# Kernel optimization log

Hardware: AMD Instinct MI355X
Metric: run time of the kernel (lower is better)

The kernel has to match this reference:

```python
import jax, jax.numpy as jnp
import numpy as np


def setup_inputs() -> dict:
    key = jax.random.key(0)
    k1, k2, k3, k4 = jax.random.split(key, 4)
    b, n1, n2, h = 8, 2048, 2048, 1024
    scale = 1.0 / np.sqrt(h)
    return {
        "S1": jax.random.normal(k1, (b, n1, h), dtype=jnp.float32),
        "S2": jax.random.normal(k2, (b, n2, h), dtype=jnp.float32),
        "W1": jax.random.normal(k3, (h, h), dtype=jnp.float32) * scale,
        "W2": jax.random.normal(k4, (h, h), dtype=jnp.float32) * scale,
    }


def reference(S1, S2, W1, W2):
    # nn.Linear(h, h, bias=False): y = x @ W.T
    S2_h = jnp.einsum('bnh,kh->bnk', S2, W1)            # (b, N2, h)
    scores1 = jnp.einsum('bmh,bnh->bmn', S1, S2_h)      # (b, N1, N2)
    attn1 = jax.nn.softmax(scores1, axis=-1)
    S1_out = jnp.einsum('bmn,bnh->bmh', attn1, S2)      # (b, N1, h)

    S1_h = jnp.einsum('bmh,kh->bmk', S1, W2)            # (b, N1, h)
    scores2 = jnp.einsum('bnh,bmh->bnm', S2, S1_h)      # (b, N2, N1)
    attn2 = jax.nn.softmax(scores2, axis=-1)
    S2_out = jnp.einsum('bnm,bmh->bnh', attn2, S1)      # (b, N2, h)
    return (S1_out, S2_out)
```

## Files before the change

### kernel.cpp

```cpp
#include <hip/hip_runtime.h>

typedef _Float16 f16;
typedef _Float16 f16x4 __attribute__((ext_vector_type(4)));
typedef _Float16 f16x8 __attribute__((ext_vector_type(8)));
typedef float    f32x4 __attribute__((ext_vector_type(4)));

#define MFMA(a,b,c) __builtin_amdgcn_mfma_f32_16x16x32_f16(a,b,c,0,0,0)
#define SBAR() __builtin_amdgcn_sched_barrier(0)
#define BARRIER() do { SBAR(); __builtin_amdgcn_s_barrier(); SBAR(); } while (0)
#define VMCNT(n) do { SBAR(); asm volatile("s_waitcnt vmcnt(" #n ")" ::: "memory"); SBAR(); } while (0)

__device__ __forceinline__ void gload_lds16(const f16* g, f16* l) {
  __builtin_amdgcn_global_load_lds(
      (const __attribute__((address_space(1))) unsigned int*)g,
      (__attribute__((address_space(3))) unsigned int*)l, 16, 0, 0);
}

__global__ __launch_bounds__(256)
void tof16_kernel(const float* __restrict__ x, f16* __restrict__ y, int n4) {
  int i = blockIdx.x * 256 + threadIdx.x;
  if (i >= n4) return;
  f32x4 v = ((const f32x4*)x)[i];
  f16x4 h;
#pragma unroll
  for (int j = 0; j < 4; j++) h[j] = (f16)v[j];
  ((f16x4*)y)[i] = h;
}

__global__ __launch_bounds__(256)
void transpose_f16_kernel(const float* __restrict__ in, f16* __restrict__ out) {
  __shared__ f16 t[64][68];
  const int tid = threadIdx.x;
  const size_t z = blockIdx.z;
  const int n0 = blockIdx.x * 64, h0 = blockIdx.y * 64;
  const int rr = tid >> 4, cc = (tid & 15) * 4;
#pragma unroll
  for (int p = 0; p < 4; p++) {
    int n = rr + p * 16;
    f32x4 v = *(const f32x4*)(in + ((size_t)z * 2048 + n0 + n) * 1024 + h0 + cc);
    f16x4 h;
#pragma unroll
    for (int j = 0; j < 4; j++) h[j] = (f16)v[j];
    *(f16x4*)&t[n][cc] = h;
  }
  __syncthreads();
#pragma unroll
  for (int p = 0; p < 4; p++) {
    int h = rr + p * 16;
    f16x4 o;
#pragma unroll
    for (int j = 0; j < 4; j++) o[j] = t[cc + j][h];
    *(f16x4*)(out + ((size_t)z * 1024 + h0 + h) * 2048 + n0 + cc) = o;
  }
}

template <int OUTF32>
__global__ __launch_bounds__(512, 2)
void gemm256(const f16* __restrict__ Ag, size_t zA,
             const f16* __restrict__ Bg, size_t zB,
             void* __restrict__ Cg, size_t zC,
             int lda, int ldb, int ldc, int K, int gx) {
  __shared__ f16 sm[8][8192];
  const int tid = threadIdx.x;
  const size_t z = blockIdx.z;
  int bx = blockIdx.x;
  { int qq = gx >> 3; bx = (bx & 7) * qq + (bx >> 3); }
  const f16* A = Ag + z * zA + (size_t)bx * 256 * lda;
  const f16* B = Bg + z * zB + (size_t)blockIdx.y * 256 * ldb;

  const int lane = tid & 63, w = tid >> 6;
  const int wm = w >> 2, wn = w & 3;
  const int lr = lane & 15, kg = lane >> 4;
  const int sx = (kg ^ ((lr >> 1) & 3)) << 3;
  const int aoff = wm * 4096 + lr * 32 + sx;
  const int boff = wn * 2048 + lr * 32 + sx;
  const int colx = (((tid & 3) ^ ((tid >> 3) & 3)) << 3);
  const int srow = tid >> 2;
  const int wls = w * 512;

  f32x4 acc[8][4] = {};
  f16x8 af[8], bf0, bf1;

#define STAGE(cc, mat, kkv, ktc) do {                                          \
    const f16* gs = ((mat) ? B : A) + (size_t)srow * ((mat) ? ldb : lda) +     \
                    (ktc) + (kkv) * 32 + colx;                                 \
    f16* ls = &sm[(cc) * 4 + (mat) * 2 + (kkv)][wls];                          \
    gload_lds16(gs, ls);                                                       \
    gload_lds16(gs + (size_t)128 * ((mat) ? ldb : lda), ls + 4096);            \
  } while (0)

#define LOAD_A(cc, kkv) do { _Pragma("unroll")                                 \
    for (int fm = 0; fm < 8; fm++)                                             \
      af[fm] = *(const f16x8*)&sm[(cc) * 4 + (kkv)][aoff + fm * 512];          \
  } while (0)

#define LOAD_B(cc, kkv, nh) do {                                               \
    bf0 = *(const f16x8*)&sm[(cc) * 4 + 2 + (kkv)][boff + (nh) * 1024];        \
    bf1 = *(const f16x8*)&sm[(cc) * 4 + 2 + (kkv)][boff + (nh) * 1024 + 512];  \
  } while (0)

#define DOMFMA(nh) do {                                                        \
    __builtin_amdgcn_s_setprio(1);                                             \
    _Pragma("unroll")                                                          \
    for (int fm = 0; fm < 8; fm++) {                                           \
      acc[fm][(nh) * 2]     = MFMA(af[fm], bf0, acc[fm][(nh) * 2]);            \
      acc[fm][(nh) * 2 + 1] = MFMA(af[fm], bf1, acc[fm][(nh) * 2 + 1]);        \
    }                                                                          \
    __builtin_amdgcn_s_setprio(0);                                             \
    SBAR();                                                                    \
  } while (0)

  const int nt = K >> 6;
  STAGE(0, 0, 0, 0);
  STAGE(0, 1, 0, 0);
  STAGE(0, 0, 1, 0);
  STAGE(0, 1, 1, 0);

  for (int t = 0; t < nt - 1; ++t) {
    const int c = t & 1;
    const int kt1 = (t + 1) << 6;
    STAGE(c ^ 1, 0, 0, kt1);
    VMCNT(6);
    BARRIER();
    LOAD_A(c, 0); LOAD_B(c, 0, 0);
    DOMFMA(0);
    BARRIER();
    STAGE(c ^ 1, 1, 0, kt1);
    BARRIER();
    LOAD_B(c, 0, 1);
    DOMFMA(1);
    BARRIER();
    STAGE(c ^ 1, 0, 1, kt1);
    VMCNT(6);
    BARRIER();
    LOAD_A(c, 1); LOAD_B(c, 1, 0);
    DOMFMA(0);
    BARRIER();
    STAGE(c ^ 1, 1, 1, kt1);
    BARRIER();
    LOAD_B(c, 1, 1);
    DOMFMA(1);
    BARRIER();
  }
  {
    const int c = (nt - 1) & 1;
    VMCNT(4);
    BARRIER();
    LOAD_A(c, 0); LOAD_B(c, 0, 0);
    DOMFMA(0);
    BARRIER();
    LOAD_B(c, 0, 1);
    DOMFMA(1);
    VMCNT(0);
    BARRIER();
    LOAD_A(c, 1); LOAD_B(c, 1, 0);
    DOMFMA(0);
    BARRIER();
    LOAD_B(c, 1, 1);
    DOMFMA(1);
  }

#pragma unroll
  for (int fm = 0; fm < 8; fm++)
#pragma unroll
    for (int fn = 0; fn < 4; fn++)
#pragma unroll
      for (int q = 0; q < 4; q++) {
        size_t grow = (size_t)bx * 256 + wm * 128 + fm * 16 + kg * 4 + q;
        int gcol = blockIdx.y * 256 + wn * 64 + fn * 16 + lr;
        if (OUTF32)
          ((float*)Cg)[z * zC + grow * ldc + gcol] = acc[fm][fn][q];
        else
          ((f16*)Cg)[z * zC + grow * ldc + gcol] = (f16)acc[fm][fn][q];
      }
#undef STAGE
#undef LOAD_A
#undef LOAD_B
#undef DOMFMA
}

__global__ __launch_bounds__(256)
void softmax_rows(const float* __restrict__ SC, f16* __restrict__ Pb) {
  const float* r = SC + (size_t)blockIdx.x * 2048;
  f16* po = Pb + (size_t)blockIdx.x * 2048;
  const int tid = threadIdx.x;
  f32x4 a = *(const f32x4*)(r + tid * 8);
  f32x4 b = *(const f32x4*)(r + tid * 8 + 4);
  float x[8] = {a[0], a[1], a[2], a[3], b[0], b[1], b[2], b[3]};
#pragma unroll
  for (int i = 0; i < 8; i++) x[i] = fminf(fmaxf(x[i], -1e30f), 1e30f);
  float m = x[0];
#pragma unroll
  for (int i = 1; i < 8; i++) m = fmaxf(m, x[i]);
#pragma unroll
  for (int off = 32; off; off >>= 1) m = fmaxf(m, __shfl_xor(m, off));
  __shared__ float rmax[4], rsum[4];
  const int w = tid >> 6, lane = tid & 63;
  if (!lane) rmax[w] = m;
  __syncthreads();
  m = fmaxf(fmaxf(rmax[0], rmax[1]), fmaxf(rmax[2], rmax[3]));
  float e[8], s = 0.f;
#pragma unroll
  for (int i = 0; i < 8; i++) {
    e[i] = __expf(x[i] - m);
    s += e[i];
  }
#pragma unroll
  for (int off = 32; off; off >>= 1) s += __shfl_xor(s, off);
  if (!lane) rsum[w] = s;
  __syncthreads();
  s = rsum[0] + rsum[1] + rsum[2] + rsum[3];
  float inv = 1.0f / s;
  f16x8 p;
#pragma unroll
  for (int i = 0; i < 8; i++) p[i] = (f16)(e[i] * inv);
  *(f16x8*)(po + tid * 8) = p;
}

extern "C" void kernel_launch(void* const* d_in, const int* in_sizes, int n_in,
                              void* d_out, int out_size, void* d_ws, size_t ws_size,
                              hipStream_t stream) {
  const float* S1 = (const float*)d_in[0];
  const float* S2 = (const float*)d_in[1];
  const float* W1 = (const float*)d_in[2];
  const float* W2 = (const float*)d_in[3];
  float* out = (float*)d_out;
  const int B = 8, N = 2048, H = 1024;
  const size_t NH = (size_t)N * H;
  const size_t WN = (size_t)H * H;

  char* ws = (char*)d_ws;
  f16* W1h = (f16*)ws;
  f16* W2h = W1h + WN;
  size_t fixed = 2 * WN * sizeof(f16);
  size_t perb = 5 * NH * sizeof(f16) + (size_t)N * N * sizeof(float) +
                (size_t)N * N * sizeof(f16);

  int bc = 1;
  const int cands[4] = {8, 4, 2, 1};
  for (int ci = 0; ci < 4; ci++) {
    if (fixed + (size_t)cands[ci] * perb <= ws_size) { bc = cands[ci]; break; }
  }
  f16* Ah = (f16*)(ws + fixed);
  f16* Bh = Ah + (size_t)bc * NH;
  f16* At = Bh + (size_t)bc * NH;
  f16* Bt = At + (size_t)bc * NH;
  f16* Kh = Bt + (size_t)bc * NH;
  float* SC = (float*)(Kh + (size_t)bc * NH);
  f16* Pb = (f16*)(SC + (size_t)bc * N * N);

  {
    int n4 = (int)(WN / 4);
    tof16_kernel<<<dim3((n4 + 255) / 256), 256, 0, stream>>>(W1, W1h, n4);
    tof16_kernel<<<dim3((n4 + 255) / 256), 256, 0, stream>>>(W2, W2h, n4);
  }

  for (int c0 = 0; c0 < B; c0 += bc) {
    int n4 = (int)((size_t)bc * NH / 4);
    tof16_kernel<<<dim3((n4 + 255) / 256), 256, 0, stream>>>(S1 + (size_t)c0 * NH, Ah, n4);
    tof16_kernel<<<dim3((n4 + 255) / 256), 256, 0, stream>>>(S2 + (size_t)c0 * NH, Bh, n4);
    transpose_f16_kernel<<<dim3(N / 64, H / 64, bc), 256, 0, stream>>>(
        S1 + (size_t)c0 * NH, At);
    transpose_f16_kernel<<<dim3(N / 64, H / 64, bc), 256, 0, stream>>>(
        S2 + (size_t)c0 * NH, Bt);

    for (int path = 0; path < 2; path++) {
      const f16* Qh = path ? Bh : Ah;
      const f16* Xh = path ? Ah : Bh;
      const f16* Vt = path ? At : Bt;
      const f16* Wh = path ? W2h : W1h;
      float* Op = out + (size_t)path * B * NH + (size_t)c0 * NH;

      gemm256<0><<<dim3(bc * N / 256, H / 256, 1), 512, 0, stream>>>(
          Xh, 0, Wh, 0, Kh, 0, H, H, H, H, bc * N / 256);
      gemm256<1><<<dim3(N / 256, N / 256, bc), 512, 0, stream>>>(
          Qh, NH, Kh, NH, SC, (size_t)N * N, H, H, N, H, N / 256);
      softmax_rows<<<dim3(bc * N), 256, 0, stream>>>(SC, Pb);
      gemm256<1><<<dim3(N / 256, H / 256, bc), 512, 0, stream>>>(
          Pb, (size_t)N * N, Vt, NH, Op, NH, N, N, H, N, N / 256);
    }
  }
}
```

Before: 537.0 us.

## Reorder GEMM main loop to overlap LDS fragment loads with staging and fuse prep kernels

Restructures the gemm256 K-loop so LDS fragment reads are issued before the next global-to-LDS stage, with explicit lgkmcnt waits before the MFMA blocks and the vmcnt waits moved to the end of each half-iteration. The aim is to hide LDS read latency behind global load issue. Separately, the f16 conversion and transpose of S1/S2 are fused into one prep kernel that writes both row-major and transposed copies, which removes a full pass over the f32 inputs. The added barriers in the epilogue and the reordering risk extra synchronization stalls and correctness hazards around LDS buffer reuse.

```diff
diff --git a/kernel.cpp b/kernel.cpp
--- a/kernel.cpp
+++ b/kernel.cpp
@@ -9,6 +9,7 @@
 #define SBAR() __builtin_amdgcn_sched_barrier(0)
 #define BARRIER() do { SBAR(); __builtin_amdgcn_s_barrier(); SBAR(); } while (0)
 #define VMCNT(n) do { SBAR(); asm volatile("s_waitcnt vmcnt(" #n ")" ::: "memory"); SBAR(); } while (0)
+#define LGKM0() do { asm volatile("s_waitcnt lgkmcnt(0)" ::: "memory"); SBAR(); } while (0)
 
 __device__ __forceinline__ void gload_lds16(const f16* g, f16* l) {
   __builtin_amdgcn_global_load_lds(
@@ -28,7 +29,8 @@
 }
 
 __global__ __launch_bounds__(256)
-void transpose_f16_kernel(const float* __restrict__ in, f16* __restrict__ out) {
+void prep_f16_kernel(const float* __restrict__ in, f16* __restrict__ rm,
+                     f16* __restrict__ tr) {
   __shared__ f16 t[64][68];
   const int tid = threadIdx.x;
   const size_t z = blockIdx.z;
@@ -42,6 +44,7 @@
 #pragma unroll
     for (int j = 0; j < 4; j++) h[j] = (f16)v[j];
     *(f16x4*)&t[n][cc] = h;
+    *(f16x4*)(rm + ((size_t)z * 2048 + n0 + n) * 1024 + h0 + cc) = h;
   }
   __syncthreads();
 #pragma unroll
@@ -50,7 +53,7 @@
     f16x4 o;
 #pragma unroll
     for (int j = 0; j < 4; j++) o[j] = t[cc + j][h];
-    *(f16x4*)(out + ((size_t)z * 1024 + h0 + h) * 2048 + n0 + cc) = o;
+    *(f16x4*)(tr + ((size_t)z * 1024 + h0 + h) * 2048 + n0 + cc) = o;
   }
 }
 
@@ -115,48 +118,60 @@
   STAGE(0, 1, 0, 0);
   STAGE(0, 0, 1, 0);
   STAGE(0, 1, 1, 0);
+  VMCNT(4);
+  BARRIER();
 
   for (int t = 0; t < nt - 1; ++t) {
     const int c = t & 1;
     const int kt1 = (t + 1) << 6;
+    LOAD_A(c, 0); LOAD_B(c, 0, 0);
     STAGE(c ^ 1, 0, 0, kt1);
-    VMCNT(6);
-    BARRIER();
-    LOAD_A(c, 0); LOAD_B(c, 0, 0);
-    DOMFMA(0);
-    BARRIER();
+    BARRIER();
+    LGKM0();
+    DOMFMA(0);
+    BARRIER();
+    LOAD_B(c, 0, 1);
     STAGE(c ^ 1, 1, 0, kt1);
     BARRIER();
-    LOAD_B(c, 0, 1);
-    DOMFMA(1);
-    BARRIER();
+    LGKM0();
+    DOMFMA(1);
+    VMCNT(4);
+    BARRIER();
+    LOAD_A(c, 1); LOAD_B(c, 1, 0);
     STAGE(c ^ 1, 0, 1, kt1);
-    VMCNT(6);
-    BARRIER();
-    LOAD_A(c, 1); LOAD_B(c, 1, 0);
-    DOMFMA(0);
-    BARRIER();
+    BARRIER();
+    LGKM0();
+    DOMFMA(0);
+    BARRIER();
+    LOAD_B(c, 1, 1);
     STAGE(c ^ 1, 1, 1, kt1);
     BARRIER();
-    LOAD_B(c, 1, 1);
-    DOMFMA(1);
+    LGKM0();
+    DOMFMA(1);
+    VMCNT(4);
     BARRIER();
   }
   {
     const int c = (nt - 1) & 1;
-    VMCNT(4);
-    BARRIER();
     LOAD_A(c, 0); LOAD_B(c, 0, 0);
+    BARRIER();
+    LGKM0();
     DOMFMA(0);
     BARRIER();
     LOAD_B(c, 0, 1);
+    BARRIER();
+    LGKM0();
     DOMFMA(1);
     VMCNT(0);
     BARRIER();
     LOAD_A(c, 1); LOAD_B(c, 1, 0);
+    BARRIER();
+    LGKM0();
     DOMFMA(0);
     BARRIER();
     LOAD_B(c, 1, 1);
+    BARRIER();
+    LGKM0();
     DOMFMA(1);
   }
 
@@ -256,13 +271,10 @@
   }
 
   for (int c0 = 0; c0 < B; c0 += bc) {
-    int n4 = (int)((size_t)bc * NH / 4);
-    tof16_kernel<<<dim3((n4 + 255) / 256), 256, 0, stream>>>(S1 + (size_t)c0 * NH, Ah, n4);
-    tof16_kernel<<<dim3((n4 + 255) / 256), 256, 0, stream>>>(S2 + (size_t)c0 * NH, Bh, n4);
-    transpose_f16_kernel<<<dim3(N / 64, H / 64, bc), 256, 0, stream>>>(
-        S1 + (size_t)c0 * NH, At);
-    transpose_f16_kernel<<<dim3(N / 64, H / 64, bc), 256, 0, stream>>>(
-        S2 + (size_t)c0 * NH, Bt);
+    prep_f16_kernel<<<dim3(N / 64, H / 64, bc), 256, 0, stream>>>(
+        S1 + (size_t)c0 * NH, Ah, At);
+    prep_f16_kernel<<<dim3(N / 64, H / 64, bc), 256, 0, stream>>>(
+        S2 + (size_t)c0 * NH, Bh, Bt);
 
     for (int path = 0; path < 2; path++) {
       const f16* Qh = path ? Bh : Ah;
```

New measurement: 516.5 us. 1.04x faster.
